# Kernel optimization log

Hardware: AMD Instinct MI355X
Metric: run time of the kernel (lower is better)

The kernel has to match this reference:

```python
import jax, jax.numpy as jnp
import numpy as np

TOP_K = 8
N_EXPERTS = 256
N_GROUP = 8
TOPK_GROUP = 4
ROUTED_SCALING = 2.5
NORM_TOPK_PROB = True
HIDDEN = 4096
TOKENS = 16384


def setup_inputs() -> dict:
    key = jax.random.key(0)
    k1, k2, k3 = jax.random.split(key, 3)
    hidden_states = jax.random.normal(k1, (TOKENS, HIDDEN), dtype=jnp.float32)
    weight = jax.random.normal(k2, (N_EXPERTS, HIDDEN), dtype=jnp.float32) * 0.02
    e_score_correction_bias = jax.random.normal(k3, (N_EXPERTS,), dtype=jnp.float32) * 0.1
    return {
        "hidden_states": hidden_states,
        "weight": weight,
        "e_score_correction_bias": e_score_correction_bias,
    }


def _get_topk_indices(scores, bias):
    # scores: [T, E]
    T = scores.shape[0]
    scores_for_choice = scores + bias[None, :]                      # [T, E]
    grp = scores_for_choice.reshape(T, N_GROUP, N_EXPERTS // N_GROUP)
    top2_vals, _ = jax.lax.top_k(grp, 2)                            # [T, G, 2]
    group_scores = top2_vals.sum(axis=-1)                           # [T, G]
    _, group_idx = jax.lax.top_k(group_scores, TOPK_GROUP)          # [T, topk_group]
    group_mask = jnp.zeros((T, N_GROUP), dtype=scores.dtype)
    group_mask = jnp.take_along_axis(group_mask, group_idx, axis=1)  # placeholder, replaced below
    # scatter 1s into selected groups
    group_mask = jnp.zeros((T, N_GROUP), dtype=bool)
    group_mask = group_mask.at[jnp.arange(T)[:, None], group_idx].set(True)
    score_mask = jnp.repeat(group_mask, N_EXPERTS // N_GROUP, axis=1)  # [T, E]
    masked = jnp.where(score_mask, scores_for_choice, 0.0)
    _, topk_indices = jax.lax.top_k(masked, TOP_K)                  # [T, top_k]
    return topk_indices


def reference(hidden_states, weight, e_score_correction_bias):
    # router logits: [T, E]
    router_logits = jnp.einsum("th,eh->te", hidden_states.astype(jnp.float32),
                               weight.astype(jnp.float32))
    scores = jax.nn.sigmoid(router_logits)
    topk_indices = _get_topk_indices(scores, e_score_correction_bias)
    topk_weights = jnp.take_along_axis(scores, topk_indices, axis=1)  # [T, top_k]
    if NORM_TOPK_PROB:
        denom = topk_weights.sum(axis=-1, keepdims=True) + 1e-20
        topk_weights = topk_weights / denom
    topk_weights = topk_weights * ROUTED_SCALING
    return topk_indices, topk_weights.astype(jnp.float32)
```

## Files before the change

### kernel.cpp

```cpp
#include <hip/hip_runtime.h>
#include <math.h>

#define T_TOKENS 16384
#define HID      4096
#define NEXP     256
#define NGROUP   8
#define GSIZE    32
#define TOPKG    4
#define TOPK     8
#define RSCALE   2.5f

#define TAU   2e-5f
#define TAUG  3e-5f

#define BM     64
#define BK     32
#define SPLITK 4
#define KSPAN  (HID / SPLITK)
#define NKS    (KSPAN / BK)
#define CSTR   136
#define TSTR   544
#define A_HI   0
#define A_LO   2176
#define B_HI   4352
#define B_LO   13056
#define STG_TOT 21760

typedef __attribute__((ext_vector_type(8))) short bf16x8;
typedef __attribute__((ext_vector_type(4))) float f32x4;

__device__ __forceinline__ int stoff(int r, int q) {
    return (r >> 4) * TSTR + (q >> 1) * CSTR + (r & 15) * 8 + (q & 1) * 4;
}
__device__ __forceinline__ int froff(int lane) {
    return (lane >> 4) * CSTR + (lane & 15) * 8;
}

__device__ __forceinline__ void split4(const float4 v, uint& h01, uint& h23,
                                       uint& l01, uint& l23) {
    const uint u0 = __float_as_uint(v.x) + 0x8000u;
    const uint u1 = __float_as_uint(v.y) + 0x8000u;
    const uint u2 = __float_as_uint(v.z) + 0x8000u;
    const uint u3 = __float_as_uint(v.w) + 0x8000u;
    h01 = __builtin_amdgcn_perm(u1, u0, 0x07060302u);
    h23 = __builtin_amdgcn_perm(u3, u2, 0x07060302u);
    const float f0 = v.x - __uint_as_float(u0 & 0xFFFF0000u);
    const float f1 = v.y - __uint_as_float(u1 & 0xFFFF0000u);
    const float f2 = v.z - __uint_as_float(u2 & 0xFFFF0000u);
    const float f3 = v.w - __uint_as_float(u3 & 0xFFFF0000u);
    l01 = __builtin_amdgcn_perm(__float_as_uint(f1) + 0x8000u,
                                __float_as_uint(f0) + 0x8000u, 0x07060302u);
    l23 = __builtin_amdgcn_perm(__float_as_uint(f3) + 0x8000u,
                                __float_as_uint(f2) + 0x8000u, 0x07060302u);
}

template <class SC>
__device__ __forceinline__ bool route_core(SC sc, const float* __restrict__ bias,
                                           int* id, float* wv)
{
    float gs[NGROUP];
#pragma unroll
    for (int g = 0; g < NGROUP; ++g) {
        float m1 = -1e30f, m2 = -1e30f;
        for (int i = 0; i < GSIZE; ++i) {
            const int e = g * GSIZE + i;
            const float v = sc(e) + bias[e];
            if (v > m1)      { m2 = m1; m1 = v; }
            else if (v > m2) { m2 = v; }
        }
        gs[g] = m1 + m2;
    }

    unsigned gmask = 0;
    float g4 = -1e30f;
#pragma unroll
    for (int r = 0; r < TOPKG; ++r) {
        int bi = 0; float bv = -1e30f;
#pragma unroll
        for (int g = 0; g < NGROUP; ++g) {
            const bool taken = (gmask >> g) & 1;
            if (!taken && gs[g] > bv) { bv = gs[g]; bi = g; }
        }
        gmask |= 1u << bi;
        g4 = bv;
    }
    float g5 = -1e30f;
#pragma unroll
    for (int g = 0; g < NGROUP; ++g)
        if (!((gmask >> g) & 1) && gs[g] > g5) g5 = gs[g];

    float val[TOPK + 1]; int vid[TOPK + 1];
#pragma unroll
    for (int r = 0; r <= TOPK; ++r) { val[r] = -1e30f; vid[r] = 0; }
    for (int e = 0; e < NEXP; ++e) {
        const bool allowed = (gmask >> (e >> 5)) & 1;
        const float v = allowed ? (sc(e) + bias[e]) : 0.0f;
        if (v > val[TOPK]) {
#pragma unroll
            for (int p = TOPK; p >= 1; --p) {
                if (v > val[p - 1])  { val[p] = val[p - 1]; vid[p] = vid[p - 1]; }
                else if (v > val[p]) { val[p] = v;          vid[p] = e; }
            }
            if (v > val[0]) { val[0] = v; vid[0] = e; }
        }
    }

    bool tight = (g4 - g5 < TAUG);
#pragma unroll
    for (int i = 0; i < TOPK; ++i) tight |= (val[i] - val[i + 1] < TAU);

    float sum = 0.0f;
#pragma unroll
    for (int r = 0; r < TOPK; ++r) { id[r] = vid[r]; wv[r] = sc(vid[r]); sum += wv[r]; }
    const float inv = RSCALE / (sum + 1e-20f);
#pragma unroll
    for (int r = 0; r < TOPK; ++r) wv[r] *= inv;
    return tight;
}

__device__ void exact_token(const float* __restrict__ hs, const float* __restrict__ wt,
                            const float* __restrict__ bias, float* __restrict__ out, int t)
{
    float lg[NEXP];
    const float* hrow = hs + (size_t)t * HID;
    for (int e = 0; e < NEXP; ++e) {
        const float* wr = wt + (size_t)e * HID;
        float a = 0.0f;
        for (int k = 0; k < HID; k += 4) {
            const float4 x = *(const float4*)(hrow + k);
            const float4 b = *(const float4*)(wr + k);
            a = fmaf(x.x, b.x, a); a = fmaf(x.y, b.y, a);
            a = fmaf(x.z, b.z, a); a = fmaf(x.w, b.w, a);
        }
        lg[e] = 1.0f / (1.0f + expf(-a));
    }
    int id[TOPK]; float wv[TOPK];
    route_core([&](int e) { return lg[e]; }, bias, id, wv);
    for (int r = 0; r < TOPK; ++r) {
        out[(size_t)t * TOPK + r] = (float)id[r];
        out[(size_t)T_TOKENS * TOPK + (size_t)t * TOPK + r] = wv[r];
    }
}

__global__ __launch_bounds__(256, 2)
void router_gemm(const float* __restrict__ hs, const float* __restrict__ wt,
                 float* __restrict__ pw)
{
    __shared__ ushort u16[STG_TOT];

    const int tid  = threadIdx.x;
    const int lane = tid & 63;
    const int w    = tid >> 6;
    const int m    = blockIdx.x >> 2;
    const int sk   = blockIdx.x & 3;
    const int t0   = m * BM;
    const int kb0  = sk * KSPAN;
    const int r0   = tid >> 3;
    const int q    = tid & 7;

    f32x4 acc[4][4];
#pragma unroll
    for (int i = 0; i < 4; ++i)
#pragma unroll
        for (int j = 0; j < 4; ++j) acc[i][j] = (f32x4)0.0f;

    float4 ra[2], rb[8];
#pragma unroll
    for (int s = 0; s < 2; ++s)
        ra[s] = *(const float4*)(hs + (size_t)(t0 + r0 + 32 * s) * HID + kb0 + q * 4);
#pragma unroll
    for (int i = 0; i < 8; ++i)
        rb[i] = *(const float4*)(wt + (size_t)(r0 + 32 * i) * HID + kb0 + q * 4);

    for (int ks = 0; ks < NKS; ++ks) {
        __syncthreads();

#pragma unroll
        for (int s = 0; s < 2; ++s) {
            const int r = r0 + 32 * s;
            uint h01, h23, l01, l23;
            split4(ra[s], h01, h23, l01, l23);
            const int eo = stoff(r, q);
            uint2 hv; hv.x = h01; hv.y = h23;
            uint2 lv; lv.x = l01; lv.y = l23;
            *(uint2*)&u16[A_HI + eo] = hv;
            *(uint2*)&u16[A_LO + eo] = lv;
        }
#pragma unroll
        for (int i = 0; i < 8; ++i) {
            const int r = r0 + 32 * i;
            uint h01, h23, l01, l23;
            split4(rb[i], h01, h23, l01, l23);
            const int eo = stoff(r, q);
            uint2 hv; hv.x = h01; hv.y = h23;
            uint2 lv; lv.x = l01; lv.y = l23;
            *(uint2*)&u16[B_HI + eo] = hv;
            *(uint2*)&u16[B_LO + eo] = lv;
        }
        __syncthreads();

        if (ks + 1 < NKS) {
            const int kb = kb0 + (ks + 1) * BK;
#pragma unroll
            for (int s = 0; s < 2; ++s)
                ra[s] = *(const float4*)(hs + (size_t)(t0 + r0 + 32 * s) * HID + kb + q * 4);
#pragma unroll
            for (int i = 0; i < 8; ++i)
                rb[i] = *(const float4*)(wt + (size_t)(r0 + 32 * i) * HID + kb + q * 4);
        }

        const int fo = froff(lane);
        bf16x8 ah[4], al[4];
#pragma unroll
        for (int rt = 0; rt < 4; ++rt) {
            ah[rt] = *(const bf16x8*)&u16[A_HI + rt * TSTR + fo];
            al[rt] = *(const bf16x8*)&u16[A_LO + rt * TSTR + fo];
        }
#pragma unroll
        for (int c = 0; c < 4; ++c) {
            const int ct = w * 4 + c;
            const bf16x8 bh = *(const bf16x8*)&u16[B_HI + ct * TSTR + fo];
            const bf16x8 bl = *(const bf16x8*)&u16[B_LO + ct * TSTR + fo];
#pragma unroll
            for (int rt = 0; rt < 4; ++rt) {
                acc[rt][c] = __builtin_amdgcn_mfma_f32_16x16x32_bf16(ah[rt], bh, acc[rt][c], 0, 0, 0);
                acc[rt][c] = __builtin_amdgcn_mfma_f32_16x16x32_bf16(ah[rt], bl, acc[rt][c], 0, 0, 0);
                acc[rt][c] = __builtin_amdgcn_mfma_f32_16x16x32_bf16(al[rt], bh, acc[rt][c], 0, 0, 0);
            }
        }
    }

#pragma unroll
    for (int rt = 0; rt < 4; ++rt)
#pragma unroll
        for (int c = 0; c < 4; ++c) {
            const int col  = w * 64 + c * 16 + (lane & 15);
            const int rowb = rt * 16 + (lane >> 4) * 4;
#pragma unroll
            for (int j = 0; j < 4; ++j)
                pw[((size_t)(sk * T_TOKENS) + t0 + rowb + j) * NEXP + col] = acc[rt][c][j];
        }
}

__global__ __launch_bounds__(256, 2)
void router_route(const float* __restrict__ pw, const float* __restrict__ bias,
                  float* __restrict__ out,
                  unsigned* __restrict__ wcnt, unsigned* __restrict__ wlist,
                  unsigned cap)
{
    __shared__ float Lg[NEXP * 64];
    const int tid = threadIdx.x;
    const int t0  = blockIdx.x * 64;

#pragma unroll 8
    for (int t = 0; t < 64; ++t) {
        float v = 0.0f;
#pragma unroll
        for (int s = 0; s < SPLITK; ++s)
            v += pw[((size_t)(s * T_TOKENS) + t0 + t) * NEXP + tid];
        Lg[tid * 64 + ((t + tid) & 63)] = 1.0f / (1.0f + expf(-v));
    }
    __syncthreads();

    if (tid < 64) {
        const int t = t0 + tid;
        int id[TOPK]; float wv[TOPK];
        const bool tight = route_core(
            [&](int e) { return Lg[e * 64 + ((tid + e) & 63)]; }, bias, id, wv);

#pragma unroll
        for (int r = 0; r < TOPK; ++r) {
            out[(size_t)t * TOPK + r] = (float)id[r];
            out[(size_t)T_TOKENS * TOPK + (size_t)t * TOPK + r] = wv[r];
        }
        if (tight) {
            const unsigned pos = atomicAdd(wcnt, 1u);
            if (pos < cap) wlist[pos] = (unsigned)t;
        }
    }
}

__global__ __launch_bounds__(256, 4)
void router_exact(const float* __restrict__ hs, const float* __restrict__ wt,
                  const float* __restrict__ bias, float* __restrict__ out,
                  const unsigned* __restrict__ wcnt, const unsigned* __restrict__ wlist,
                  unsigned cap)
{
    __shared__ float hrow[HID];
    __shared__ float lg[NEXP];
    const unsigned count = min(*wcnt, cap);
    const int tid  = threadIdx.x;
    const int lane = tid & 63;
    const int w    = tid >> 6;

    for (unsigned b = blockIdx.x; b < count; b += gridDim.x) {
        __syncthreads();
        const int t = (int)wlist[b];

#pragma unroll
        for (int i = 0; i < 4; ++i) {
            const int f4 = i * 256 + tid;
            *(float4*)&hrow[f4 * 4] = *(const float4*)(hs + (size_t)t * HID + f4 * 4);
        }
        __syncthreads();

        for (int g = 0; g < 16; ++g) {
            const int e0 = w * 64 + g * 4;
            float a[4] = {0.0f, 0.0f, 0.0f, 0.0f};
#pragma unroll 4
            for (int j = 0; j < 16; ++j) {
                const int f4 = j * 64 + lane;
                const float4 h = *(const float4*)&hrow[f4 * 4];
#pragma unroll
                for (int p = 0; p < 4; ++p) {
                    const float4 v = *(const float4*)(wt + (size_t)(e0 + p) * HID + f4 * 4);
                    a[p] = fmaf(h.x, v.x, a[p]); a[p] = fmaf(h.y, v.y, a[p]);
                    a[p] = fmaf(h.z, v.z, a[p]); a[p] = fmaf(h.w, v.w, a[p]);
                }
            }
#pragma unroll
            for (int p = 0; p < 4; ++p)
#pragma unroll
                for (int d = 1; d < 64; d <<= 1)
                    a[p] += __shfl_xor(a[p], d, 64);
            if (lane == 0) {
#pragma unroll
                for (int p = 0; p < 4; ++p)
                    lg[e0 + p] = 1.0f / (1.0f + expf(-a[p]));
            }
        }
        __syncthreads();

        if (tid == 0) {
            int id[TOPK]; float wv[TOPK];
            route_core([&](int e) { return lg[e]; }, bias, id, wv);
            for (int r = 0; r < TOPK; ++r) {
                out[(size_t)t * TOPK + r] = (float)id[r];
                out[(size_t)T_TOKENS * TOPK + (size_t)t * TOPK + r] = wv[r];
            }
        }
    }
}

__global__ __launch_bounds__(512, 1)
void router_mono(const float* __restrict__ hs, const float* __restrict__ wt,
                 const float* __restrict__ bias, float* __restrict__ out,
                 unsigned* __restrict__ wcnt, unsigned* __restrict__ wlist, unsigned cap)
{
    __shared__ float smem[16384];
    ushort* u16 = (ushort*)smem;
    float*  Lg  = smem;

    const int tid  = threadIdx.x;
    const int lane = tid & 63;
    const int w    = tid >> 6;
    const int t0   = blockIdx.x * 64;
    const int ar   = tid >> 3;
    const int aq   = tid & 7;

    f32x4 acc[4][2];
#pragma unroll
    for (int i = 0; i < 4; ++i)
#pragma unroll
        for (int j = 0; j < 2; ++j) acc[i][j] = (f32x4)0.0f;

    float4 ra, rb[4];
    ra = *(const float4*)(hs + (size_t)(t0 + ar) * HID + aq * 4);
#pragma unroll
    for (int s = 0; s < 4; ++s)
        rb[s] = *(const float4*)(wt + (size_t)(ar + s * 64) * HID + aq * 4);

    for (int ks = 0; ks < HID / BK; ++ks) {
        __syncthreads();
        {
            uint h01, h23, l01, l23;
            split4(ra, h01, h23, l01, l23);
            const int eo = (ar >> 4) * 512 + (aq >> 1) * 128 + (ar & 15) * 8 + (aq & 1) * 4;
            uint2 hv; hv.x = h01; hv.y = h23;
            uint2 lv; lv.x = l01; lv.y = l23;
            *(uint2*)&u16[0 + eo] = hv;
            *(uint2*)&u16[2048 + eo] = lv;
        }
#pragma unroll
        for (int s = 0; s < 4; ++s) {
            const int e = ar + s * 64;
            uint h01, h23, l01, l23;
            split4(rb[s], h01, h23, l01, l23);
            const int eo = (e >> 4) * 512 + (aq >> 1) * 128 + (e & 15) * 8 + (aq & 1) * 4;
            uint2 hv; hv.x = h01; hv.y = h23;
            uint2 lv; lv.x = l01; lv.y = l23;
            *(uint2*)&u16[4096 + eo] = hv;
            *(uint2*)&u16[12288 + eo] = lv;
        }
        __syncthreads();
        if (ks + 1 < HID / BK) {
            const int k0 = (ks + 1) * BK;
            ra = *(const float4*)(hs + (size_t)(t0 + ar) * HID + k0 + aq * 4);
#pragma unroll
            for (int s = 0; s < 4; ++s)
                rb[s] = *(const float4*)(wt + (size_t)(ar + s * 64) * HID + k0 + aq * 4);
        }
        bf16x8 ah[4], al[4];
#pragma unroll
        for (int rt = 0; rt < 4; ++rt) {
            ah[rt] = *(const bf16x8*)&u16[0 + rt * 512 + lane * 8];
            al[rt] = *(const bf16x8*)&u16[2048 + rt * 512 + lane * 8];
        }
#pragma unroll
        for (int c = 0; c < 2; ++c) {
            const int ct = w * 2 + c;
            const bf16x8 bh = *(const bf16x8*)&u16[4096 + ct * 512 + lane * 8];
            const bf16x8 bl = *(const bf16x8*)&u16[12288 + ct * 512 + lane * 8];
#pragma unroll
            for (int rt = 0; rt < 4; ++rt) {
                acc[rt][c] = __builtin_amdgcn_mfma_f32_16x16x32_bf16(ah[rt], bh, acc[rt][c], 0, 0, 0);
                acc[rt][c] = __builtin_amdgcn_mfma_f32_16x16x32_bf16(ah[rt], bl, acc[rt][c], 0, 0, 0);
                acc[rt][c] = __builtin_amdgcn_mfma_f32_16x16x32_bf16(al[rt], bh, acc[rt][c], 0, 0, 0);
            }
        }
    }
    __syncthreads();
#pragma unroll
    for (int rt = 0; rt < 4; ++rt)
#pragma unroll
        for (int c = 0; c < 2; ++c) {
            const int col  = w * 32 + c * 16 + (lane & 15);
            const int rowb = rt * 16 + (lane >> 4) * 4;
#pragma unroll
            for (int j = 0; j < 4; ++j) {
                const int row = rowb + j;
                Lg[col * 64 + ((row + col) & 63)] = 1.0f / (1.0f + expf(-acc[rt][c][j]));
            }
        }
    __syncthreads();

    if (tid < 64) {
        const int t = t0 + tid;
        int id[TOPK]; float wv[TOPK];
        const bool tight = route_core(
            [&](int e) { return Lg[e * 64 + ((tid + e) & 63)]; }, bias, id, wv);
#pragma unroll
        for (int r = 0; r < TOPK; ++r) {
            out[(size_t)t * TOPK + r] = (float)id[r];
            out[(size_t)T_TOKENS * TOPK + (size_t)t * TOPK + r] = wv[r];
        }
        if (tight) {
            bool queued = false;
            if (wcnt) {
                const unsigned pos = atomicAdd(wcnt, 1u);
                if (pos < cap) { wlist[pos] = (unsigned)t; queued = true; }
            }
            if (!queued) exact_token(hs, wt, bias, out, t);
        }
    }
}

extern "C" void kernel_launch(void* const* d_in, const int* in_sizes, int n_in,
                              void* d_out, int out_size, void* d_ws, size_t ws_size,
                              hipStream_t stream) {
    const float* hs   = (const float*)d_in[0];
    const float* wt   = (const float*)d_in[1];
    const float* bias = (const float*)d_in[2];
    float* out = (float*)d_out;
    (void)in_sizes; (void)n_in; (void)out_size;

    const size_t PW_BYTES = (size_t)SPLITK * T_TOKENS * NEXP * 4;
    const size_t NEED = PW_BYTES + 4 + (size_t)T_TOKENS * 4;

    if (ws_size >= NEED) {
        float*    pw    = (float*)d_ws;
        unsigned* wcnt  = (unsigned*)((char*)d_ws + PW_BYTES);
        unsigned* wlist = wcnt + 1;
        hipMemsetAsync(wcnt, 0, sizeof(unsigned), stream);
        router_gemm<<<(T_TOKENS / BM) * SPLITK, 256, 0, stream>>>(hs, wt, pw);
        router_route<<<T_TOKENS / 64, 256, 0, stream>>>(pw, bias, out, wcnt, wlist,
                                                        (unsigned)T_TOKENS);
        router_exact<<<2048, 256, 0, stream>>>(hs, wt, bias, out, wcnt, wlist,
                                               (unsigned)T_TOKENS);
    } else if (ws_size >= 8) {
        unsigned cap = (unsigned)((ws_size - 4) / 4);
        if (cap > T_TOKENS) cap = T_TOKENS;
        unsigned* wcnt  = (unsigned*)d_ws;
        unsigned* wlist = wcnt + 1;
        hipMemsetAsync(d_ws, 0, sizeof(unsigned), stream);
        router_mono<<<T_TOKENS / 64, 512, 0, stream>>>(hs, wt, bias, out, wcnt, wlist, cap);
        router_exact<<<2048, 256, 0, stream>>>(hs, wt, bias, out, wcnt, wlist, cap);
    } else {
        router_mono<<<T_TOKENS / 64, 512, 0, stream>>>(hs, wt, bias, out,
                                                       nullptr, nullptr, 0u);
    }
}
```

Measured before the change: 353.1 us.

## Pre-split weight into bf16 hi/lo tiles and stream via direct global-to-LDS loads

A new pre-pass kernel converts the fp32 router weight once per call into bf16 hi/lo limbs, stored in the exact tiled LDS layout. The GEMM then fetches weight tiles with global_load_lds directly into shared memory. This removes the per-block weight split work and the register staging, and frees enough registers to raise launch bounds to 4 blocks per SM. The padded LDS stride is dropped in favour of the unpadded layout, which risks bank conflicts. The extra kernel launch also adds workspace traffic, and the weight loads are no longer software-prefetched one step ahead.

```diff
diff --git a/kernel.cpp b/kernel.cpp
--- a/kernel.cpp
+++ b/kernel.cpp
@@ -18,22 +18,30 @@
 #define SPLITK 4
 #define KSPAN  (HID / SPLITK)
 #define NKS    (KSPAN / BK)
-#define CSTR   136
-#define TSTR   544
+#define NSG    (HID / BK)
+
 #define A_HI   0
-#define A_LO   2176
-#define B_HI   4352
-#define B_LO   13056
-#define STG_TOT 21760
+#define A_LO   2048
+#define B_HI   4096
+#define B_LO   12288
+#define STG_TOT 20480
+
+#define WQ_LIMB (NSG * 8192)
 
 typedef __attribute__((ext_vector_type(8))) short bf16x8;
 typedef __attribute__((ext_vector_type(4))) float f32x4;
 
-__device__ __forceinline__ int stoff(int r, int q) {
-    return (r >> 4) * TSTR + (q >> 1) * CSTR + (r & 15) * 8 + (q & 1) * 4;
-}
-__device__ __forceinline__ int froff(int lane) {
-    return (lane >> 4) * CSTR + (lane & 15) * 8;
+__device__ __forceinline__ int stoffA(int r, int q) {
+    return (r >> 4) * 512 + (q >> 1) * 128 + (r & 15) * 8 + (q & 1) * 4;
+}
+__device__ __forceinline__ int froffL(int lane) {
+    return (lane >> 4) * 128 + (lane & 15) * 8;
+}
+
+__device__ __forceinline__ void gload16(const void* g, void* l) {
+    __builtin_amdgcn_global_load_lds(
+        (const __attribute__((address_space(1))) void*)g,
+        (__attribute__((address_space(3))) void*)l, 16, 0, 0);
 }
 
 __device__ __forceinline__ void split4(const float4 v, uint& h01, uint& h23,
@@ -142,8 +150,30 @@
     }
 }
 
-__global__ __launch_bounds__(256, 2)
-void router_gemm(const float* __restrict__ hs, const float* __restrict__ wt,
+__global__ __launch_bounds__(256, 8)
+void conv_weight(const float* __restrict__ wt, ushort* __restrict__ wq)
+{
+    const int g  = blockIdx.x * 256 + threadIdx.x;
+    const int e  = g >> 9;
+    const int kc = g & 511;
+    const int sg  = kc >> 2;
+    const int kch = kc & 3;
+
+    const float4 v0 = *(const float4*)(wt + (size_t)e * HID + kc * 8);
+    const float4 v1 = *(const float4*)(wt + (size_t)e * HID + kc * 8 + 4);
+    uint h01, h23, l01, l23, h45, h67, l45, l67;
+    split4(v0, h01, h23, l01, l23);
+    split4(v1, h45, h67, l45, l67);
+
+    const size_t idx = (size_t)sg * 8192 + (size_t)((e >> 4) * 512 + kch * 128 + (e & 15) * 8);
+    uint4 hv; hv.x = h01; hv.y = h23; hv.z = h45; hv.w = h67;
+    uint4 lv; lv.x = l01; lv.y = l23; lv.z = l45; lv.w = l67;
+    *(uint4*)&wq[idx] = hv;
+    *(uint4*)&wq[(size_t)WQ_LIMB + idx] = lv;
+}
+
+__global__ __launch_bounds__(256, 4)
+void router_gemm(const float* __restrict__ hs, const ushort* __restrict__ wq,
                  float* __restrict__ pw)
 {
     __shared__ ushort u16[STG_TOT];
@@ -158,45 +188,43 @@
     const int r0   = tid >> 3;
     const int q    = tid & 7;
 
+    const ushort* wq_hi = wq;
+    const ushort* wq_lo = wq + WQ_LIMB;
+
     f32x4 acc[4][4];
 #pragma unroll
     for (int i = 0; i < 4; ++i)
 #pragma unroll
         for (int j = 0; j < 4; ++j) acc[i][j] = (f32x4)0.0f;
 
-    float4 ra[2], rb[8];
+    float4 ra[2];
 #pragma unroll
     for (int s = 0; s < 2; ++s)
         ra[s] = *(const float4*)(hs + (size_t)(t0 + r0 + 32 * s) * HID + kb0 + q * 4);
-#pragma unroll
-    for (int i = 0; i < 8; ++i)
-        rb[i] = *(const float4*)(wt + (size_t)(r0 + 32 * i) * HID + kb0 + q * 4);
 
     for (int ks = 0; ks < NKS; ++ks) {
-        __syncthreads();
-
+        const int sg = sk * NKS + ks;
+        __syncthreads();
+
+        {
+            const size_t gb = (size_t)sg * 8192 + (size_t)(w * 4) * 512 + (size_t)lane * 8;
+#pragma unroll
+            for (int i = 0; i < 4; ++i) {
+                gload16(wq_hi + gb + i * 512, &u16[B_HI + (w * 4 + i) * 512]);
+                gload16(wq_lo + gb + i * 512, &u16[B_LO + (w * 4 + i) * 512]);
+            }
+        }
 #pragma unroll
         for (int s = 0; s < 2; ++s) {
             const int r = r0 + 32 * s;
             uint h01, h23, l01, l23;
             split4(ra[s], h01, h23, l01, l23);
-            const int eo = stoff(r, q);
+            const int eo = stoffA(r, q);
             uint2 hv; hv.x = h01; hv.y = h23;
             uint2 lv; lv.x = l01; lv.y = l23;
             *(uint2*)&u16[A_HI + eo] = hv;
             *(uint2*)&u16[A_LO + eo] = lv;
         }
-#pragma unroll
-        for (int i = 0; i < 8; ++i) {
-            const int r = r0 + 32 * i;
-            uint h01, h23, l01, l23;
-            split4(rb[i], h01, h23, l01, l23);
-            const int eo = stoff(r, q);
-            uint2 hv; hv.x = h01; hv.y = h23;
-            uint2 lv; lv.x = l01; lv.y = l23;
-            *(uint2*)&u16[B_HI + eo] = hv;
-            *(uint2*)&u16[B_LO + eo] = lv;
-        }
         __syncthreads();
 
         if (ks + 1 < NKS) {
@@ -204,23 +232,20 @@
 #pragma unroll
             for (int s = 0; s < 2; ++s)
                 ra[s] = *(const float4*)(hs + (size_t)(t0 + r0 + 32 * s) * HID + kb + q * 4);
-#pragma unroll
-            for (int i = 0; i < 8; ++i)
-                rb[i] = *(const float4*)(wt + (size_t)(r0 + 32 * i) * HID + kb + q * 4);
-        }
-
-        const int fo = froff(lane);
+        }
+
+        const int fo = froffL(lane);
         bf16x8 ah[4], al[4];
 #pragma unroll
         for (int rt = 0; rt < 4; ++rt) {
-            ah[rt] = *(const bf16x8*)&u16[A_HI + rt * TSTR + fo];
-            al[rt] = *(const bf16x8*)&u16[A_LO + rt * TSTR + fo];
+            ah[rt] = *(const bf16x8*)&u16[A_HI + rt * 512 + fo];
+            al[rt] = *(const bf16x8*)&u16[A_LO + rt * 512 + fo];
         }
 #pragma unroll
         for (int c = 0; c < 4; ++c) {
             const int ct = w * 4 + c;
-            const bf16x8 bh = *(const bf16x8*)&u16[B_HI + ct * TSTR + fo];
-            const bf16x8 bl = *(const bf16x8*)&u16[B_LO + ct * TSTR + fo];
+            const bf16x8 bh = *(const bf16x8*)&u16[B_HI + ct * 512 + fo];
+            const bf16x8 bl = *(const bf16x8*)&u16[B_LO + ct * 512 + fo];
 #pragma unroll
             for (int rt = 0; rt < 4; ++rt) {
                 acc[rt][c] = __builtin_amdgcn_mfma_f32_16x16x32_bf16(ah[rt], bh, acc[rt][c], 0, 0, 0);
@@ -375,7 +400,7 @@
         {
             uint h01, h23, l01, l23;
             split4(ra, h01, h23, l01, l23);
-            const int eo = (ar >> 4) * 512 + (aq >> 1) * 128 + (ar & 15) * 8 + (aq & 1) * 4;
+            const int eo = stoffA(ar, aq);
             uint2 hv; hv.x = h01; hv.y = h23;
             uint2 lv; lv.x = l01; lv.y = l23;
             *(uint2*)&u16[0 + eo] = hv;
@@ -386,7 +411,7 @@
             const int e = ar + s * 64;
             uint h01, h23, l01, l23;
             split4(rb[s], h01, h23, l01, l23);
-            const int eo = (e >> 4) * 512 + (aq >> 1) * 128 + (e & 15) * 8 + (aq & 1) * 4;
+            const int eo = stoffA(e, aq);
             uint2 hv; hv.x = h01; hv.y = h23;
             uint2 lv; lv.x = l01; lv.y = l23;
             *(uint2*)&u16[4096 + eo] = hv;
@@ -400,17 +425,18 @@
             for (int s = 0; s < 4; ++s)
                 rb[s] = *(const float4*)(wt + (size_t)(ar + s * 64) * HID + k0 + aq * 4);
         }
+        const int fo = froffL(lane);
         bf16x8 ah[4], al[4];
 #pragma unroll
         for (int rt = 0; rt < 4; ++rt) {
-            ah[rt] = *(const bf16x8*)&u16[0 + rt * 512 + lane * 8];
-            al[rt] = *(const bf16x8*)&u16[2048 + rt * 512 + lane * 8];
+            ah[rt] = *(const bf16x8*)&u16[0 + rt * 512 + fo];
+            al[rt] = *(const bf16x8*)&u16[2048 + rt * 512 + fo];
         }
 #pragma unroll
         for (int c = 0; c < 2; ++c) {
             const int ct = w * 2 + c;
-            const bf16x8 bh = *(const bf16x8*)&u16[4096 + ct * 512 + lane * 8];
-            const bf16x8 bl = *(const bf16x8*)&u16[12288 + ct * 512 + lane * 8];
+            const bf16x8 bh = *(const bf16x8*)&u16[4096 + ct * 512 + fo];
+            const bf16x8 bl = *(const bf16x8*)&u16[12288 + ct * 512 + fo];
 #pragma unroll
             for (int rt = 0; rt < 4; ++rt) {
                 acc[rt][c] = __builtin_amdgcn_mfma_f32_16x16x32_bf16(ah[rt], bh, acc[rt][c], 0, 0, 0);
@@ -465,14 +491,17 @@
     (void)in_sizes; (void)n_in; (void)out_size;
 
     const size_t PW_BYTES = (size_t)SPLITK * T_TOKENS * NEXP * 4;
-    const size_t NEED = PW_BYTES + 4 + (size_t)T_TOKENS * 4;
+    const size_t WQ_BYTES = (size_t)2 * WQ_LIMB * 2;
+    const size_t NEED = PW_BYTES + WQ_BYTES + 4 + (size_t)T_TOKENS * 4;
 
     if (ws_size >= NEED) {
         float*    pw    = (float*)d_ws;
-        unsigned* wcnt  = (unsigned*)((char*)d_ws + PW_BYTES);
+        ushort*   wq    = (ushort*)((char*)d_ws + PW_BYTES);
+        unsigned* wcnt  = (unsigned*)((char*)d_ws + PW_BYTES + WQ_BYTES);
         unsigned* wlist = wcnt + 1;
         hipMemsetAsync(wcnt, 0, sizeof(unsigned), stream);
-        router_gemm<<<(T_TOKENS / BM) * SPLITK, 256, 0, stream>>>(hs, wt, pw);
+        conv_weight<<<512, 256, 0, stream>>>(wt, wq);
+        router_gemm<<<(T_TOKENS / BM) * SPLITK, 256, 0, stream>>>(hs, wq, pw);
         router_route<<<T_TOKENS / 64, 256, 0, stream>>>(pw, bias, out, wcnt, wlist,
                                                         (unsigned)T_TOKENS);
         router_exact<<<2048, 256, 0, stream>>>(hs, wt, bias, out, wcnt, wlist,
```

After: 357.2 us. Within noise of the previous version (+1.2%).
